# Optimization experiments

Hardware: AMD Instinct MI355X
Metric: run time of the kernel (lower is better)

## Reference

```python
import jax, jax.numpy as jnp
import numpy as np

EPS = 1e-5
NEG_SLOPE = 0.1


def setup_inputs() -> dict:
    key = jax.random.key(0)
    ks = jax.random.split(key, 4)
    B, Cin, Cout, D, E, EMB = 2, 32, 32, 40, 3, 1
    return {
        "x": jax.random.normal(ks[0], (B, Cin, D, D, D), dtype=jnp.float32),
        "embedding": jax.random.normal(ks[1], (B, EMB), dtype=jnp.float32),
        "route_w": jax.random.normal(ks[2], (EMB, E), dtype=jnp.float32),
        "route_b": jnp.zeros((E,), dtype=jnp.float32),
        "expert_kernels": jax.random.normal(ks[3], (E, Cout, Cin, 3, 3, 3), dtype=jnp.float32) * 0.05,
        "expert_bias": jnp.zeros((E, Cout), dtype=jnp.float32),
        "gamma": jnp.ones((Cout,), dtype=jnp.float32),
        "beta": jnp.zeros((Cout,), dtype=jnp.float32),
    }


def reference(x, embedding, route_w, route_b, expert_kernels, expert_bias, gamma, beta):
    # CondConv routing: sigmoid(Linear(embedding)) -> per-sample expert weights [B, E]
    r = jax.nn.sigmoid(embedding @ route_w + route_b)
    # Per-sample combined kernel [B, O, I, 3, 3, 3] and bias [B, O]
    w = jnp.einsum('be,eoixyz->boixyz', r, expert_kernels)
    b = r @ expert_bias

    def conv_one(xi, wi):
        # xi: [Cin, D, H, W], wi: [O, I, 3, 3, 3] -> [Cout, D, H, W]
        return jax.lax.conv_general_dilated(
            xi[None], wi, window_strides=(1, 1, 1), padding='SAME',
            dimension_numbers=('NCDHW', 'OIDHW', 'NCDHW'))[0]

    y = jax.vmap(conv_one)(x, w) + b[:, :, None, None, None]  # [B, O, D, H, W]

    # BatchNorm3d (training mode: biased batch stats over B,D,H,W per channel)
    mean = jnp.mean(y, axis=(0, 2, 3, 4), keepdims=True)
    var = jnp.mean(jnp.square(y - mean), axis=(0, 2, 3, 4), keepdims=True)
    y = (y - mean) * jax.lax.rsqrt(var + EPS)
    y = y * gamma[None, :, None, None, None] + beta[None, :, None, None, None]

    # LeakyReLU(0.1)
    y = jnp.where(y >= 0, y, NEG_SLOPE * y)

    # Upsample nearest, scale_factor=2 on all 3 spatial dims
    y = jnp.repeat(jnp.repeat(jnp.repeat(y, 2, axis=2), 2, axis=3), 2, axis=4)
    return y
```

## Files before the change

kernel.cpp:

```cpp
#include <hip/hip_runtime.h>
#include <hip/hip_bf16.h>
#include <math.h>

#define BB   2
#define CIN  32
#define COUT 32
#define DM   40
#define PD   42
#define NPTS (DM*DM)
#define NVOL (DM*DM*DM)
#define EPSBN 1e-5f
#define NBLK_CONV 4000

typedef short  bf16x8  __attribute__((ext_vector_type(8)));
typedef float  floatx4 __attribute__((ext_vector_type(4)));

#define WS_WFRAG 0
#define WS_BCOMB 27648
#define WS_SC    27712
#define WS_SH    27744
#define WS_PART  27776
#define WS_XPAD2 283776
#define WS_Y     2654592

__global__ void prep_kernel(const float* __restrict__ emb,
                            const float* __restrict__ rw,
                            const float* __restrict__ rb,
                            const float* __restrict__ ek,
                            const float* __restrict__ ebias,
                            float* __restrict__ ws) {
    int idx = blockIdx.x * 256 + threadIdx.x;
    __hip_bfloat16* wfrag = (__hip_bfloat16*)(ws + WS_WFRAG);
    const int NW = 2 * 2 * 27 * 64 * 8;
    if (idx < NW) {
        int j    = idx & 7;
        int lane = (idx >> 3) & 63;
        int tap  = (idx >> 9) % 27;
        int nt   = (idx / (27 * 512)) & 1;
        int b    = idx / (2 * 27 * 512);
        int o = nt * 16 + (lane & 15);
        int i = (lane >> 4) * 8 + j;
        float e0 = emb[b];
        float w = 0.0f;
        #pragma unroll
        for (int e = 0; e < 3; ++e) {
            float r = 1.0f / (1.0f + expf(-(e0 * rw[e] + rb[e])));
            w += r * ek[((e * COUT + o) * CIN + i) * 27 + tap];
        }
        wfrag[idx] = __float2bfloat16(w);
    } else if (idx < NW + 64) {
        int j2 = idx - NW;
        int b = j2 >> 5, o = j2 & 31;
        float e0 = emb[b];
        float bv = 0.0f;
        #pragma unroll
        for (int e = 0; e < 3; ++e) {
            float r = 1.0f / (1.0f + expf(-(e0 * rw[e] + rb[e])));
            bv += r * ebias[e * COUT + o];
        }
        ws[WS_BCOMB + j2] = bv;
    }
}

__global__ void repack_kernel(const float* __restrict__ x,
                              __hip_bfloat16* __restrict__ xp2) {
    int yp = blockIdx.x, zp = blockIdx.y, b = blockIdx.z;
    __hip_bfloat16* row = xp2 + ((((size_t)b * PD + zp) * PD + yp) * PD) * 32;
    bool inz = (zp >= 1 && zp <= DM && yp >= 1 && yp <= DM);
    for (int idx = threadIdx.x; idx < PD * 32; idx += 256) {
        int i = idx & 31, xp = idx >> 5;
        float v = 0.0f;
        if (inz && xp >= 1 && xp <= DM)
            v = x[(size_t)(b * CIN + i) * NVOL + (zp - 1) * NPTS + (yp - 1) * DM + (xp - 1)];
        row[idx] = __float2bfloat16(v);
    }
}

__global__ __launch_bounds__(256, 2) void conv_mfma_kernel(
        const __hip_bfloat16* __restrict__ xp2,
        const bf16x8* __restrict__ wfrag,
        const float* __restrict__ bcomb,
        float* __restrict__ y,
        float* __restrict__ part) {
    const int mc = blockIdx.x, z = blockIdx.y, b = blockIdx.z;
    const int tid = threadIdx.x, lane = tid & 63, wv = tid >> 6;
    const int mt = wv & 1, nt = wv >> 1;
    const int quad = lane >> 4, l15 = lane & 15;

    __shared__ float lstat[64];
    if (tid < 64) lstat[tid] = 0.0f;
    __syncthreads();

    const int pa = mc * 32 + mt * 16 + l15;
    const int ya = pa / DM, xa = pa % DM;
    const char* abase = (const char*)xp2 +
        ((((size_t)b * PD + z) * PD + ya) * PD + xa) * 64 + quad * 16;
    const bf16x8* wbase = wfrag + ((b * 2 + nt) * 27) * 64 + lane;

    floatx4 acc0 = {0.f, 0.f, 0.f, 0.f};
    floatx4 acc1 = {0.f, 0.f, 0.f, 0.f};
    #pragma unroll
    for (int t = 0; t < 27; ++t) {
        const int dz = t / 9, dy = (t / 3) % 3, dx = t % 3;
        bf16x8 av = *(const bf16x8*)(abase + ((dz * PD + dy) * PD + dx) * 64);
        bf16x8 bv = wbase[t * 64];
        if (t & 1) acc1 = __builtin_amdgcn_mfma_f32_16x16x32_bf16(av, bv, acc1, 0, 0, 0);
        else       acc0 = __builtin_amdgcn_mfma_f32_16x16x32_bf16(av, bv, acc0, 0, 0, 0);
    }
    floatx4 acc = acc0 + acc1;

    const int o = nt * 16 + l15;
    const float bias = bcomb[b * COUT + o];
    const int po = mc * 32 + mt * 16 + quad * 4;
    float v0 = acc[0] + bias;
    float v1 = acc[1] + bias;
    float v2 = acc[2] + bias;
    float v3 = acc[3] + bias;
    float vs = v0 + v1 + v2 + v3;
    float vq = v0 * v0 + v1 * v1 + v2 * v2 + v3 * v3;
    atomicAdd(&lstat[o],      vs);
    atomicAdd(&lstat[32 + o], vq);
    *(float4*)(y + ((size_t)(b * COUT + o) * DM + z) * NPTS + po) =
        make_float4(v0, v1, v2, v3);

    __syncthreads();
    if (tid < 64) {
        int blin = (b * DM + z) * 50 + mc;
        part[tid * NBLK_CONV + blin] = lstat[tid];
    }
}

__global__ void finalize_kernel(const float* __restrict__ part,
                                const float* __restrict__ gamma,
                                const float* __restrict__ beta,
                                float* __restrict__ sc,
                                float* __restrict__ sh) {
    int c = blockIdx.x, tid = threadIdx.x;
    float s1 = 0.f, s2 = 0.f;
    for (int k = tid; k < NBLK_CONV; k += 256) {
        s1 += part[c * NBLK_CONV + k];
        s2 += part[(32 + c) * NBLK_CONV + k];
    }
    __shared__ float r1[256], r2[256];
    r1[tid] = s1; r2[tid] = s2;
    __syncthreads();
    for (int s = 128; s > 0; s >>= 1) {
        if (tid < s) { r1[tid] += r1[tid + s]; r2[tid] += r2[tid + s]; }
        __syncthreads();
    }
    if (tid == 0) {
        const float invN = 1.0f / (float)(BB * NVOL);
        float mean = r1[0] * invN;
        float var  = r2[0] * invN - mean * mean;
        float scale = gamma[c] * rsqrtf(var + EPSBN);
        sc[c] = scale;
        sh[c] = beta[c] - mean * scale;
    }
}

__global__ void upsample_kernel(const float* __restrict__ yin,
                                const float* __restrict__ sc,
                                const float* __restrict__ sh,
                                float* __restrict__ out) {
    int idx = blockIdx.x * blockDim.x + threadIdx.x;
    if (idx >= BB * COUT * NVOL) return;
    int x = idx % DM;
    int y = (idx / DM) % DM;
    int z = (idx / NPTS) % DM;
    int c = (idx / NVOL) % COUT;
    int cc = idx / NVOL;

    float v = yin[idx];
    v = v * sc[c] + sh[c];
    v = (v >= 0.0f) ? v : 0.1f * v;

    float2 vv = make_float2(v, v);
    size_t obase = ((size_t)cc * 80 + (size_t)(2 * z)) * 6400
                 + (size_t)(2 * y) * 80 + (size_t)(2 * x);
    *(float2*)(out + obase)            = vv;
    *(float2*)(out + obase + 80)       = vv;
    *(float2*)(out + obase + 6400)     = vv;
    *(float2*)(out + obase + 6480)     = vv;
}

extern "C" void kernel_launch(void* const* d_in, const int* in_sizes, int n_in,
                              void* d_out, int out_size, void* d_ws, size_t ws_size,
                              hipStream_t stream) {
    const float* x     = (const float*)d_in[0];
    const float* emb   = (const float*)d_in[1];
    const float* rw    = (const float*)d_in[2];
    const float* rb    = (const float*)d_in[3];
    const float* ek    = (const float*)d_in[4];
    const float* ebias = (const float*)d_in[5];
    const float* gamma = (const float*)d_in[6];
    const float* beta  = (const float*)d_in[7];
    float* ws  = (float*)d_ws;
    float* out = (float*)d_out;

    __hip_bfloat16* xp2 = (__hip_bfloat16*)(ws + WS_XPAD2);

    prep_kernel<<<(55296 + 64 + 255) / 256, 256, 0, stream>>>(emb, rw, rb, ek, ebias, ws);

    repack_kernel<<<dim3(PD, PD, BB), 256, 0, stream>>>(x, xp2);

    conv_mfma_kernel<<<dim3(50, DM, BB), 256, 0, stream>>>(
        xp2, (const bf16x8*)(ws + WS_WFRAG), ws + WS_BCOMB, ws + WS_Y, ws + WS_PART);

    finalize_kernel<<<32, 256, 0, stream>>>(ws + WS_PART, gamma, beta,
                                            ws + WS_SC, ws + WS_SH);

    upsample_kernel<<<(BB * COUT * NVOL + 255) / 256, 256, 0, stream>>>(
        ws + WS_Y, ws + WS_SC, ws + WS_SH, out);
}
```

Before: 215.8 us.

## Merge prep/repack, use global atomics for BN stats, fold finalize into upsample

Merges the weight-prep and input-repack kernels into one launch, and has that launch zero a 64-float stats buffer. Conv blocks now pre-reduce their BN sums across the wavefront with shuffles and atomically add them into the global buffer, which removes the partials array and the separate finalize kernel. The upsample kernel computes scale and shift per block from the sums and handles two inputs per thread with float4 stores. This cuts two kernel launches and reduces reduction traffic, at the cost of global atomic contention and float accumulation whose order is no longer deterministic.

```diff
diff --git a/kernel.cpp b/kernel.cpp
--- a/kernel.cpp
+++ b/kernel.cpp
@@ -10,26 +10,46 @@
 #define NPTS (DM*DM)
 #define NVOL (DM*DM*DM)
 #define EPSBN 1e-5f
-#define NBLK_CONV 4000
 
 typedef short  bf16x8  __attribute__((ext_vector_type(8)));
 typedef float  floatx4 __attribute__((ext_vector_type(4)));
 
 #define WS_WFRAG 0
 #define WS_BCOMB 27648
-#define WS_SC    27712
-#define WS_SH    27744
-#define WS_PART  27776
-#define WS_XPAD2 283776
-#define WS_Y     2654592
-
-__global__ void prep_kernel(const float* __restrict__ emb,
-                            const float* __restrict__ rw,
-                            const float* __restrict__ rb,
-                            const float* __restrict__ ek,
-                            const float* __restrict__ ebias,
-                            float* __restrict__ ws) {
-    int idx = blockIdx.x * 256 + threadIdx.x;
+#define WS_SUM   27712
+#define WS_XPAD2 27776
+#define WS_Y     2398592
+
+#define REPACK_BLOCKS (PD*PD*BB)
+#define PREP_ELEMS    (55296 + 64 + 64)
+#define PREP_BLOCKS   ((PREP_ELEMS + 255) / 256)
+
+__global__ void prep_repack_kernel(const float* __restrict__ x,
+                                   const float* __restrict__ emb,
+                                   const float* __restrict__ rw,
+                                   const float* __restrict__ rb,
+                                   const float* __restrict__ ek,
+                                   const float* __restrict__ ebias,
+                                   float* __restrict__ ws) {
+    const int bid = blockIdx.x;
+    if (bid < REPACK_BLOCKS) {
+        int b  = bid / (PD * PD);
+        int r  = bid % (PD * PD);
+        int zp = r / PD, yp = r % PD;
+        __hip_bfloat16* row = (__hip_bfloat16*)(ws + WS_XPAD2) +
+                              ((((size_t)b * PD + zp) * PD + yp) * PD) * 32;
+        bool inz = (zp >= 1 && zp <= DM && yp >= 1 && yp <= DM);
+        for (int idx = threadIdx.x; idx < PD * 32; idx += 256) {
+            int i = idx & 31, xp = idx >> 5;
+            float v = 0.0f;
+            if (inz && xp >= 1 && xp <= DM)
+                v = x[(size_t)(b * CIN + i) * NVOL +
+                      (zp - 1) * NPTS + (yp - 1) * DM + (xp - 1)];
+            row[idx] = __float2bfloat16(v);
+        }
+        return;
+    }
+    int idx = (bid - REPACK_BLOCKS) * 256 + threadIdx.x;
     __hip_bfloat16* wfrag = (__hip_bfloat16*)(ws + WS_WFRAG);
     const int NW = 2 * 2 * 27 * 64 * 8;
     if (idx < NW) {
@@ -59,29 +79,17 @@
             bv += r * ebias[e * COUT + o];
         }
         ws[WS_BCOMB + j2] = bv;
-    }
-}
-
-__global__ void repack_kernel(const float* __restrict__ x,
-                              __hip_bfloat16* __restrict__ xp2) {
-    int yp = blockIdx.x, zp = blockIdx.y, b = blockIdx.z;
-    __hip_bfloat16* row = xp2 + ((((size_t)b * PD + zp) * PD + yp) * PD) * 32;
-    bool inz = (zp >= 1 && zp <= DM && yp >= 1 && yp <= DM);
-    for (int idx = threadIdx.x; idx < PD * 32; idx += 256) {
-        int i = idx & 31, xp = idx >> 5;
-        float v = 0.0f;
-        if (inz && xp >= 1 && xp <= DM)
-            v = x[(size_t)(b * CIN + i) * NVOL + (zp - 1) * NPTS + (yp - 1) * DM + (xp - 1)];
-        row[idx] = __float2bfloat16(v);
-    }
-}
-
-__global__ __launch_bounds__(256, 2) void conv_mfma_kernel(
+    } else if (idx < NW + 128) {
+        ws[WS_SUM + (idx - NW - 64)] = 0.0f;
+    }
+}
+
+__global__ __launch_bounds__(256) void conv_mfma_kernel(
         const __hip_bfloat16* __restrict__ xp2,
         const bf16x8* __restrict__ wfrag,
         const float* __restrict__ bcomb,
         float* __restrict__ y,
-        float* __restrict__ part) {
+        float* __restrict__ sums) {
     const int mc = blockIdx.x, z = blockIdx.y, b = blockIdx.z;
     const int tid = threadIdx.x, lane = tid & 63, wv = tid >> 6;
     const int mt = wv & 1, nt = wv >> 1;
@@ -116,71 +124,58 @@
     float v1 = acc[1] + bias;
     float v2 = acc[2] + bias;
     float v3 = acc[3] + bias;
+    *(float4*)(y + ((size_t)(b * COUT + o) * DM + z) * NPTS + po) =
+        make_float4(v0, v1, v2, v3);
+
     float vs = v0 + v1 + v2 + v3;
     float vq = v0 * v0 + v1 * v1 + v2 * v2 + v3 * v3;
-    atomicAdd(&lstat[o],      vs);
-    atomicAdd(&lstat[32 + o], vq);
-    *(float4*)(y + ((size_t)(b * COUT + o) * DM + z) * NPTS + po) =
-        make_float4(v0, v1, v2, v3);
-
+    vs += __shfl_xor(vs, 16); vq += __shfl_xor(vq, 16);
+    vs += __shfl_xor(vs, 32); vq += __shfl_xor(vq, 32);
+    if (lane < 16) {
+        atomicAdd(&lstat[o],      vs);
+        atomicAdd(&lstat[32 + o], vq);
+    }
     __syncthreads();
-    if (tid < 64) {
-        int blin = (b * DM + z) * 50 + mc;
-        part[tid * NBLK_CONV + blin] = lstat[tid];
-    }
-}
-
-__global__ void finalize_kernel(const float* __restrict__ part,
+    if (tid < 64) atomicAdd(&sums[tid], lstat[tid]);
+}
+
+__global__ void upsample_kernel(const float* __restrict__ yin,
+                                const float* __restrict__ sums,
                                 const float* __restrict__ gamma,
                                 const float* __restrict__ beta,
-                                float* __restrict__ sc,
-                                float* __restrict__ sh) {
-    int c = blockIdx.x, tid = threadIdx.x;
-    float s1 = 0.f, s2 = 0.f;
-    for (int k = tid; k < NBLK_CONV; k += 256) {
-        s1 += part[c * NBLK_CONV + k];
-        s2 += part[(32 + c) * NBLK_CONV + k];
-    }
-    __shared__ float r1[256], r2[256];
-    r1[tid] = s1; r2[tid] = s2;
+                                float* __restrict__ out) {
+    __shared__ float ssc[32], ssh[32];
+    const int tid = threadIdx.x;
+    if (tid < 32) {
+        const float invN = 1.0f / (float)(BB * NVOL);
+        float mean  = sums[tid] * invN;
+        float var   = sums[32 + tid] * invN - mean * mean;
+        float scale = gamma[tid] * rsqrtf(var + EPSBN);
+        ssc[tid] = scale;
+        ssh[tid] = beta[tid] - mean * scale;
+    }
     __syncthreads();
-    for (int s = 128; s > 0; s >>= 1) {
-        if (tid < s) { r1[tid] += r1[tid + s]; r2[tid] += r2[tid + s]; }
-        __syncthreads();
-    }
-    if (tid == 0) {
-        const float invN = 1.0f / (float)(BB * NVOL);
-        float mean = r1[0] * invN;
-        float var  = r2[0] * invN - mean * mean;
-        float scale = gamma[c] * rsqrtf(var + EPSBN);
-        sc[c] = scale;
-        sh[c] = beta[c] - mean * scale;
-    }
-}
-
-__global__ void upsample_kernel(const float* __restrict__ yin,
-                                const float* __restrict__ sc,
-                                const float* __restrict__ sh,
-                                float* __restrict__ out) {
-    int idx = blockIdx.x * blockDim.x + threadIdx.x;
-    if (idx >= BB * COUT * NVOL) return;
-    int x = idx % DM;
-    int y = (idx / DM) % DM;
-    int z = (idx / NPTS) % DM;
-    int c = (idx / NVOL) % COUT;
-    int cc = idx / NVOL;
-
-    float v = yin[idx];
-    v = v * sc[c] + sh[c];
-    v = (v >= 0.0f) ? v : 0.1f * v;
-
-    float2 vv = make_float2(v, v);
+
+    int idx = blockIdx.x * 256 + tid;
+    int cc = idx / (NVOL / 2);
+    int p  = idx % (NVOL / 2);
+    int z  = p / (NPTS / 2);
+    int yy = (p / (DM / 2)) % DM;
+    int x2 = p % (DM / 2);
+    int c  = cc & 31;
+
+    float2 v = *(const float2*)(yin + (size_t)idx * 2);
+    float sc = ssc[c], sh = ssh[c];
+    float w0 = v.x * sc + sh; w0 = (w0 >= 0.0f) ? w0 : 0.1f * w0;
+    float w1 = v.y * sc + sh; w1 = (w1 >= 0.0f) ? w1 : 0.1f * w1;
+
+    float4 q = make_float4(w0, w0, w1, w1);
     size_t obase = ((size_t)cc * 80 + (size_t)(2 * z)) * 6400
-                 + (size_t)(2 * y) * 80 + (size_t)(2 * x);
-    *(float2*)(out + obase)            = vv;
-    *(float2*)(out + obase + 80)       = vv;
-    *(float2*)(out + obase + 6400)     = vv;
-    *(float2*)(out + obase + 6480)     = vv;
+                 + (size_t)(2 * yy) * 80 + (size_t)(4 * x2);
+    *(float4*)(out + obase)        = q;
+    *(float4*)(out + obase + 80)   = q;
+    *(float4*)(out + obase + 6400) = q;
+    *(float4*)(out + obase + 6480) = q;
 }
 
 extern "C" void kernel_launch(void* const* d_in, const int* in_sizes, int n_in,
@@ -197,18 +192,13 @@
     float* ws  = (float*)d_ws;
     float* out = (float*)d_out;
 
-    __hip_bfloat16* xp2 = (__hip_bfloat16*)(ws + WS_XPAD2);
-
-    prep_kernel<<<(55296 + 64 + 255) / 256, 256, 0, stream>>>(emb, rw, rb, ek, ebias, ws);
-
-    repack_kernel<<<dim3(PD, PD, BB), 256, 0, stream>>>(x, xp2);
+    prep_repack_kernel<<<REPACK_BLOCKS + PREP_BLOCKS, 256, 0, stream>>>(
+        x, emb, rw, rb, ek, ebias, ws);
 
     conv_mfma_kernel<<<dim3(50, DM, BB), 256, 0, stream>>>(
-        xp2, (const bf16x8*)(ws + WS_WFRAG), ws + WS_BCOMB, ws + WS_Y, ws + WS_PART);
-
-    finalize_kernel<<<32, 256, 0, stream>>>(ws + WS_PART, gamma, beta,
-                                            ws + WS_SC, ws + WS_SH);
-
-    upsample_kernel<<<(BB * COUT * NVOL + 255) / 256, 256, 0, stream>>>(
-        ws + WS_Y, ws + WS_SC, ws + WS_SH, out);
-}
+        (const __hip_bfloat16*)(ws + WS_XPAD2), (const bf16x8*)(ws + WS_WFRAG),
+        ws + WS_BCOMB, ws + WS_Y, ws + WS_SUM);
+
+    upsample_kernel<<<(BB * COUT * NVOL / 2) / 256, 256, 0, stream>>>(
+        ws + WS_Y, ws + WS_SUM, gamma, beta, out);
+}
```

After: 268.8 us. 24.5% more time.
